# Kernel tuning notes

Measured on AMD Instinct MI355X. Metric: run time of the kernel, lower is better.

The kernel has to match this reference:

```python
import jax, jax.numpy as jnp
import numpy as np

B, T, OBS, ACT, H, S = 512, 64, 1024, 32, 1024, 64


def setup_inputs() -> dict:
    key = jax.random.key(0)
    ks = jax.random.split(key, 16)
    w = lambda k, shape: 0.02 * jax.random.normal(k, shape, jnp.float32)
    return {
        "obs": jax.random.normal(ks[0], (B, T, OBS), jnp.float32),
        "action": jax.random.normal(ks[1], (B, T, ACT), jnp.float32),
        "eps": jax.random.normal(ks[2], (B, T, S), jnp.float32),
        # obs encoder: Linear(OBS->H) + ReLU
        "W_enc": w(ks[3], (H, OBS)), "b_enc": jnp.zeros((H,), jnp.float32),
        # GRUCell(stoch+action -> H), torch gate order: r, z, n
        "W_ih": w(ks[4], (3 * H, S + ACT)), "W_hh": w(ks[5], (3 * H, H)),
        "b_ih": jnp.zeros((3 * H,), jnp.float32), "b_hh": jnp.zeros((3 * H,), jnp.float32),
        # prior: Linear(H -> 2S); posterior: Linear(2H -> 2S)
        "W_prior": w(ks[6], (2 * S, H)), "b_prior": jnp.zeros((2 * S,), jnp.float32),
        "W_post": w(ks[7], (2 * S, 2 * H)), "b_post": jnp.zeros((2 * S,), jnp.float32),
        # decoder: Linear(H+S -> H) ReLU Linear(H -> OBS)
        "W_dec1": w(ks[8], (H, H + S)), "b_dec1": jnp.zeros((H,), jnp.float32),
        "W_dec2": w(ks[9], (OBS, H)), "b_dec2": jnp.zeros((OBS,), jnp.float32),
        # reward / done heads: Linear(H+S -> 1)
        "W_rew": w(ks[10], (1, H + S)), "b_rew": jnp.zeros((1,), jnp.float32),
        "W_done": w(ks[11], (1, H + S)), "b_done": jnp.zeros((1,), jnp.float32),
    }


def _stats(x):
    mean, raw_std = jnp.split(x, 2, axis=-1)
    return mean, jax.nn.softplus(raw_std) + 1e-4


def reference(obs, action, eps, W_enc, b_enc, W_ih, W_hh, b_ih, b_hh,
              W_prior, b_prior, W_post, b_post, W_dec1, b_dec1, W_dec2, b_dec2,
              W_rew, b_rew, W_done, b_done):
    batch = obs.shape[0]
    hid = W_hh.shape[1]
    sdim = eps.shape[-1]
    # obs encoder is per-step independent -> batch it over time up front
    emb_all = jax.nn.relu(jnp.einsum('bto,ho->bth', obs, W_enc) + b_enc)

    def step(carry, xs):
        deter, stoch = carry
        a_t, emb_t, eps_t = xs
        # torch GRUCell
        x = jnp.concatenate([stoch, a_t], axis=-1)
        gi = x @ W_ih.T + b_ih
        gh = deter @ W_hh.T + b_hh
        i_r, i_z, i_n = jnp.split(gi, 3, axis=-1)
        h_r, h_z, h_n = jnp.split(gh, 3, axis=-1)
        r = jax.nn.sigmoid(i_r + h_r)
        z = jax.nn.sigmoid(i_z + h_z)
        n = jnp.tanh(i_n + r * h_n)
        deter = (1.0 - z) * n + z * deter
        # prior / posterior stats
        p_mean, p_std = _stats(deter @ W_prior.T + b_prior)
        q_mean, q_std = _stats(jnp.concatenate([deter, emb_t], axis=-1) @ W_post.T + b_post)
        stoch = q_mean + eps_t * q_std  # reparam sample
        feat = jnp.concatenate([deter, stoch], axis=-1)
        pred = jax.nn.relu(feat @ W_dec1.T + b_dec1) @ W_dec2.T + b_dec2
        rew = feat @ W_rew.T + b_rew
        done = feat @ W_done.T + b_done
        kl = jnp.log(p_std / q_std) + (q_std ** 2 + (q_mean - p_mean) ** 2) / (2.0 * p_std ** 2) - 0.5
        return (deter, stoch), (pred, rew, done, kl.mean(axis=-1, keepdims=True))

    init = (jnp.zeros((batch, hid), obs.dtype), jnp.zeros((batch, sdim), obs.dtype))
    xs = (jnp.swapaxes(action, 0, 1), jnp.swapaxes(emb_all, 0, 1), jnp.swapaxes(eps, 0, 1))
    _, (preds, rews, dones, kls) = jax.lax.scan(step, init, xs)
    pred = jnp.swapaxes(preds, 0, 1)    # [B,T,OBS]
    reward = jnp.swapaxes(rews, 0, 1)   # [B,T,1]
    done = jnp.swapaxes(dones, 0, 1)    # [B,T,1]
    kl = kls.mean()
    return pred, reward, done, kl
```

## Files before the change

kernel.cpp:

```cpp
#include <hip/hip_runtime.h>
#include <stdint.h>

#define BB 512
#define TT 64
#define OBSD 1024
#define ACTD 32
#define HD 1024
#define SD 64
#define BT (BB*TT)
#define G3 (3*HD)
#define STRD ((long)TT*HD)

typedef unsigned int uint32;
typedef unsigned long long ull;
typedef unsigned short u16;
typedef __attribute__((ext_vector_type(8))) short bf16x8;
typedef __attribute__((ext_vector_type(4))) float f32x4;

__device__ __forceinline__ float bf2f(u16 v){ uint32_t u = ((uint32_t)v)<<16; return __builtin_bit_cast(float,u); }
__device__ __forceinline__ u16 f2bf(float f){ uint32_t u = __builtin_bit_cast(uint32_t,f); uint32_t r = (u + 0x7FFFu + ((u>>16)&1u))>>16; return (u16)r; }
__device__ __forceinline__ float sigm(float x){ return 1.f/(1.f+expf(-x)); }
#define MFMA __builtin_amdgcn_mfma_f32_16x16x32_bf16

__global__ void cvt_kernel(const float* __restrict__ in, u16* __restrict__ out, long n){
  long i = (long)blockIdx.x*blockDim.x + threadIdx.x;
  long st = (long)gridDim.x*blockDim.x;
  for (; i<n; i+=st) out[i] = f2bf(in[i]);
}

struct GemmP {
  const u16* a0; const u16* a1; const u16* a2;
  const u16* b0; const u16* b1; const u16* b2;
  long lda0, lda1, lda2, ldb0, ldb1, ldb2;
  int kc0, kc1, kc2, kcPerZ;
  float* cf; u16* cb;
  long ldc, ldcb, zstride;
  const float* bias0; const float* bias1;
  int relu;
};

template<int BM,int BN>
__global__ __launch_bounds__(256) void gemm_bf16(GemmP p){
  constexpr int SA = 40;
  __shared__ u16 sA[BM*SA];
  __shared__ u16 sB[BN*SA];
  const int m0 = blockIdx.y*BM, n0 = blockIdx.x*BN;
  const int tid = threadIdx.x, lane = tid&63, wave = tid>>6;
  const int wm = (wave>>1)*(BM/2), wn = (wave&1)*(BN/2);
  constexpr int FM = BM/32, FN = BN/32;
  f32x4 acc[FM][FN] = {};
  const int cbeg = blockIdx.z*p.kcPerZ;
  int cend = cbeg + p.kcPerZ; if (cend > p.kc2) cend = p.kc2;
  const int sr = tid>>2, sc = (tid&3)*8;
  const int kg = lane>>4, lr = lane&15;
  for (int c=cbeg;c<cend;++c){
    const u16* ap; const u16* bp; long lda, ldb; int kofs;
    if (c < p.kc0){ ap=p.a0; bp=p.b0; lda=p.lda0; ldb=p.ldb0; kofs=c*32; }
    else if (c < p.kc1){ ap=p.a1; bp=p.b1; lda=p.lda1; ldb=p.ldb1; kofs=(c-p.kc0)*32; }
    else { ap=p.a2; bp=p.b2; lda=p.lda2; ldb=p.ldb2; kofs=(c-p.kc1)*32; }
    #pragma unroll
    for (int it=0; it<BM/64; ++it){
      int row = sr + it*64;
      *(bf16x8*)&sA[row*SA+sc] = *(const bf16x8*)(ap + (long)(m0+row)*lda + kofs + sc);
    }
    #pragma unroll
    for (int it=0; it<BN/64; ++it){
      int row = sr + it*64;
      *(bf16x8*)&sB[row*SA+sc] = *(const bf16x8*)(bp + (long)(n0+row)*ldb + kofs + sc);
    }
    __syncthreads();
    bf16x8 af[FM], bfv[FN];
    #pragma unroll
    for (int i=0;i<FM;++i) af[i] = *(const bf16x8*)&sA[(wm+i*16+lr)*SA + kg*8];
    #pragma unroll
    for (int j=0;j<FN;++j) bfv[j] = *(const bf16x8*)&sB[(wn+j*16+lr)*SA + kg*8];
    #pragma unroll
    for (int i=0;i<FM;++i)
      #pragma unroll
      for (int j=0;j<FN;++j)
        acc[i][j] = MFMA(af[i], bfv[j], acc[i][j], 0,0,0);
    __syncthreads();
  }
  const bool partial = (gridDim.z > 1);
  float* cf = p.cf ? (p.cf + (partial ? (long)blockIdx.z*p.zstride : 0)) : nullptr;
  #pragma unroll
  for (int i=0;i<FM;++i){
    #pragma unroll
    for (int j=0;j<FN;++j){
      const int gr0 = m0 + wm + i*16 + kg*4;
      const int gc = n0 + wn + j*16 + lr;
      float bias = 0.f;
      if (!partial){
        if (p.bias0) bias += p.bias0[gc];
        if (p.bias1) bias += p.bias1[gc];
      }
      #pragma unroll
      for (int r=0;r<4;++r){
        float v = acc[i][j][r] + bias;
        if (p.relu) v = fmaxf(v, 0.f);
        const long row = gr0 + r;
        if (cf) cf[row*p.ldc + gc] = v;
        if (p.cb) p.cb[row*p.ldcb + gc] = f2bf(v);
      }
    }
  }
}

struct ScanArgs {
  const u16* act; const u16* Wih; const u16* Whh;
  const float* b_ih; const float* b_hh;
  const u16* Wpos; const float* qemb; const float* eps;
  u16* det; u16* sto; float* qm; float* qs;
  uint32* slots;
};

__device__ __forceinline__ void gsync_g(uint32* slots, int m, int n, uint32 val){
  asm volatile("s_waitcnt vmcnt(0)" ::: "memory");
  __syncthreads();
  if (threadIdx.x == 0)
    __hip_atomic_store(&slots[m*64 + n], val, __ATOMIC_RELAXED, __HIP_MEMORY_SCOPE_AGENT);
  if (threadIdx.x < 32){
    while (__hip_atomic_load(&slots[m*64 + threadIdx.x], __ATOMIC_RELAXED,
                             __HIP_MEMORY_SCOPE_AGENT) < val)
      __builtin_amdgcn_s_sleep(2);
  }
  __syncthreads();
}

#define SA2 152

__global__ __launch_bounds__(256, 1) void scan_kernel(ScanArgs A){
  __shared__ __align__(16) u16 lds[(64+96)*SA2];
  u16* sA = lds; u16* sB = lds + 64*SA2;
  float* pf = (float*)lds;
  const int bid = blockIdx.x;
  const int tid = threadIdx.x, lane = tid&63, wave = tid>>6;
  const int lr = lane&15, kg = lane>>4;
  const int n = bid&31, m = bid>>5;
  const int m0 = m*64, h0 = n*32;
  const int wrow = (wave&1)*32, wcol = (wave>>1)*16;

  const int srow = tid>>4;
  const int scu  = (tid&15)*8;

  long whhb[6], wihb[6];
  #pragma unroll
  for (int i=0;i<6;++i){
    int br = srow + i*16;
    int gate = br>>5, hr = br&31;
    whhb[i] = (long)(gate*HD + h0 + hr)*HD + scu;
    wihb[i] = (long)(gate*HD + h0 + hr)*96 + scu;
  }

  const int h4 = h0 + wcol + kg*4;
  float bir[4], bhr[4], biz[4], bhz[4], bin[4], bhn[4];
  #pragma unroll
  for (int r=0;r<4;++r){
    bir[r]=A.b_ih[h4+r];      bhr[r]=A.b_hh[h4+r];
    biz[r]=A.b_ih[HD+h4+r];   bhz[r]=A.b_hh[HD+h4+r];
    bin[r]=A.b_ih[2*HD+h4+r]; bhn[r]=A.b_hh[2*HD+h4+r];
  }

  const int pj = n & 3, prt = n >> 2;

  float dreg[2][4] = {{0.f,0.f,0.f,0.f},{0.f,0.f,0.f,0.f}};
  const bf16x8 zerov = {};

  bf16x8 pa[4], pb[6];
  auto loadgt = [&](int tt, int g){
    if (g < 8){
      if (tt > 0){
        const u16* s = A.det + (long)(tt-1)*HD + g*128 + scu;
        #pragma unroll
        for (int j=0;j<4;++j) pa[j] = *(const bf16x8*)(s + (long)(m0+srow+16*j)*STRD);
      } else { pa[0]=zerov; pa[1]=zerov; pa[2]=zerov; pa[3]=zerov; }
      #pragma unroll
      for (int i=0;i<6;++i) pb[i] = *(const bf16x8*)(A.Whh + whhb[i] + g*128);
    } else {
      if (scu < 64){
        if (tt > 0){
          #pragma unroll
          for (int j=0;j<4;++j)
            pa[j] = *(const bf16x8*)(A.sto + (long)(m0+srow+16*j)*((long)TT*SD) + (long)(tt-1)*SD + scu);
        } else { pa[0]=zerov; pa[1]=zerov; pa[2]=zerov; pa[3]=zerov; }
      } else if (scu < 96){
        #pragma unroll
        for (int j=0;j<4;++j)
          pa[j] = *(const bf16x8*)(A.act + (long)(m0+srow+16*j)*((long)TT*ACTD) + (long)tt*ACTD + (scu-64));
      } else { pa[0]=zerov; pa[1]=zerov; pa[2]=zerov; pa[3]=zerov; }
      #pragma unroll
      for (int i=0;i<6;++i) pb[i] = (scu < 96) ? *(const bf16x8*)(A.Wih + wihb[i]) : zerov;
    }
  };

  loadgt(0, 0);
  for (int t=0; t<TT; ++t){
    f32x4 aR[2]={}, aZ[2]={}, aNd[2]={}, aNx[2]={};
    for (int g=0; g<9; ++g){
      __syncthreads();
      #pragma unroll
      for (int j=0;j<4;++j) *(bf16x8*)&sA[(srow+16*j)*SA2 + scu] = pa[j];
      #pragma unroll
      for (int i=0;i<6;++i) *(bf16x8*)&sB[(srow+16*i)*SA2 + scu] = pb[i];
      if (g < 8) loadgt(t, g+1);
      __syncthreads();
      #pragma unroll
      for (int k=0;k<4;++k){
        bf16x8 a0v = *(const bf16x8*)&sA[(wrow+lr)*SA2 + k*32 + kg*8];
        bf16x8 a1v = *(const bf16x8*)&sA[(wrow+16+lr)*SA2 + k*32 + kg*8];
        bf16x8 b0 = *(const bf16x8*)&sB[(wcol+lr)*SA2 + k*32 + kg*8];
        bf16x8 b1 = *(const bf16x8*)&sB[(32+wcol+lr)*SA2 + k*32 + kg*8];
        bf16x8 b2 = *(const bf16x8*)&sB[(64+wcol+lr)*SA2 + k*32 + kg*8];
        aR[0] = MFMA(b0,a0v,aR[0],0,0,0); aR[1] = MFMA(b0,a1v,aR[1],0,0,0);
        aZ[0] = MFMA(b1,a0v,aZ[0],0,0,0); aZ[1] = MFMA(b1,a1v,aZ[1],0,0,0);
        if (g<8){ aNd[0] = MFMA(b2,a0v,aNd[0],0,0,0); aNd[1] = MFMA(b2,a1v,aNd[1],0,0,0); }
        else    { aNx[0] = MFMA(b2,a0v,aNx[0],0,0,0); aNx[1] = MFMA(b2,a1v,aNx[1],0,0,0); }
      }
    }
    #pragma unroll
    for (int rf=0;rf<2;++rf){
      const long brow = m0 + wrow + rf*16 + lr;
      u16 pk[4];
      #pragma unroll
      for (int r=0;r<4;++r){
        float rr = sigm(aR[rf][r]+bir[r]+bhr[r]);
        float z  = sigm(aZ[rf][r]+biz[r]+bhz[r]);
        float nn = tanhf(aNx[rf][r]+bin[r] + rr*(aNd[rf][r]+bhn[r]));
        float d = (1.f - z)*nn + z*dreg[rf][r];
        dreg[rf][r] = d;
        pk[r] = f2bf(d);
      }
      ull pv; __builtin_memcpy(&pv, pk, 8);
      __hip_atomic_store((ull*)(A.det + brow*STRD + (long)t*HD + h4), pv,
                         __ATOMIC_RELAXED, __HIP_MEMORY_SCOPE_AGENT);
    }
    gsync_g(A.slots, m, n, (uint32)(2*t+1));
    {
      f32x4 accM = {}, accS = {};
      const int k0 = wave*256;
      const u16* arow = A.det + (long)(m0 + prt*8 + (lr&7))*STRD + (long)t*HD + k0 + kg*8;
      const u16* bm = A.Wpos + (long)(pj*16 + lr)*(2*HD) + k0 + kg*8;
      const u16* bs = A.Wpos + (long)(64 + pj*16 + lr)*(2*HD) + k0 + kg*8;
      #pragma unroll
      for (int kk=0; kk<8; ++kk){
        bf16x8 af = *(const bf16x8*)(arow + kk*32);
        accM = MFMA(af, *(const bf16x8*)(bm + kk*32), accM, 0,0,0);
        accS = MFMA(af, *(const bf16x8*)(bs + kk*32), accS, 0,0,0);
      }
      #pragma unroll
      for (int r=0;r<4;++r){
        int rowt = kg*4 + r;
        pf[wave*512 + rowt*16 + lr]       = accM[r];
        pf[wave*512 + 256 + rowt*16 + lr] = accS[r];
      }
      __syncthreads();
      if (tid < 64){
        const int row = tid>>3;
        const int s2 = (tid&7)*2;
        const long grow = m0 + prt*8 + row;
        const float* qe = A.qemb + grow*((long)TT*128) + (long)t*128;
        const float* ep = A.eps  + grow*((long)TT*SD) + (long)t*SD;
        u16 spk[2];
        #pragma unroll
        for (int i=0;i<2;++i){
          int sl = s2 + i, sg = pj*16 + sl;
          float mean = pf[row*16+sl] + pf[512+row*16+sl] + pf[1024+row*16+sl] + pf[1536+row*16+sl];
          float rsv  = pf[256+row*16+sl] + pf[768+row*16+sl] + pf[1280+row*16+sl] + pf[1792+row*16+sl];
          mean += qe[sg];
          rsv  += qe[64+sg];
          float sp = fmaxf(rsv,0.f) + log1pf(expf(-fabsf(rsv)));
          float qs_ = sp + 1e-4f;
          float st = mean + ep[sg]*qs_;
          A.qm[grow*((long)TT*SD) + (long)t*SD + sg] = mean;
          A.qs[grow*((long)TT*SD) + (long)t*SD + sg] = qs_;
          spk[i] = f2bf(st);
        }
        uint32 pv; __builtin_memcpy(&pv, spk, 4);
        __hip_atomic_store((uint32*)(A.sto + grow*((long)TT*SD) + (long)t*SD + pj*16 + s2), pv,
                           __ATOMIC_RELAXED, __HIP_MEMORY_SCOPE_AGENT);
      }
      __syncthreads();
    }
    if (t+1 < TT) loadgt(t+1, 0);
    gsync_g(A.slots, m, n, (uint32)(2*t+2));
  }
}

__global__ __launch_bounds__(256) void gru_step(
    const u16* __restrict__ sto_prev, long ssto,
    const u16* __restrict__ act_t,
    const u16* __restrict__ det_prev, long sdet,
    const u16* __restrict__ Wih, const u16* __restrict__ Whh,
    const float* __restrict__ b_ih, const float* __restrict__ b_hh,
    float* __restrict__ deterF, u16* __restrict__ det_bf_t){
  constexpr int SA = 40;
  __shared__ u16 sA[32*SA];
  __shared__ u16 sB[96*SA];
  const int id = blockIdx.x;
  const int n = (id&7) + ((id>>7)<<3);
  const int m = (id>>3)&15;
  const int m0 = m*32, h0 = n*32;
  const int tid = threadIdx.x, lane = tid&63, wave = tid>>6;
  const int wm = wave>>1, wn = wave&1;
  const int lr = lane&15, kg = lane>>4;

  f32x4 aR = {}, aZ = {}, aNd = {}, aNx = {};

  auto aAddr = [&](int c, int row, int sc)->const u16*{
    if (c < 32) return det_prev + (long)(m0+row)*sdet + c*32 + sc;
    if (c < 34) return sto_prev + (long)(m0+row)*ssto + (c-32)*32 + sc;
    return act_t + (long)(m0+row)*((long)TT*ACTD) + sc;
  };
  auto bAddr = [&](int c, int l)->const u16*{
    int row = l>>2, sc = (l&3)*8;
    int g = row>>5, hr = row&31;
    if (c < 32) return Whh + (long)(g*1024 + h0 + hr)*HD + c*32 + sc;
    return Wih + (long)(g*1024 + h0 + hr)*(SD+ACTD) + (c-32)*32 + sc;
  };

  bf16x8 rA, rB0, rB1;
  auto loadc = [&](int c){
    rB0 = *(const bf16x8*)bAddr(c, tid);
    if (tid < 128){
      rA  = *(const bf16x8*)aAddr(c, tid>>2, (tid&3)*8);
      rB1 = *(const bf16x8*)bAddr(c, 256+tid);
    }
  };

  loadc(0);
  for (int c=0; c<35; ++c){
    *(bf16x8*)&sB[(tid>>2)*SA + (tid&3)*8] = rB0;
    if (tid < 128){
      *(bf16x8*)&sA[(tid>>2)*SA + (tid&3)*8] = rA;
      int l = 256+tid;
      *(bf16x8*)&sB[(l>>2)*SA + (l&3)*8] = rB1;
    }
    if (c < 34) loadc(c+1);
    __syncthreads();
    bf16x8 af = *(const bf16x8*)&sA[(wm*16+lr)*SA + kg*8];
    bf16x8 b0 = *(const bf16x8*)&sB[(     wn*16+lr)*SA + kg*8];
    bf16x8 b1 = *(const bf16x8*)&sB[(32 + wn*16+lr)*SA + kg*8];
    bf16x8 b2 = *(const bf16x8*)&sB[(64 + wn*16+lr)*SA + kg*8];
    aR = MFMA(af,b0,aR,0,0,0);
    aZ = MFMA(af,b1,aZ,0,0,0);
    if (c < 32) aNd = MFMA(af,b2,aNd,0,0,0);
    else        aNx = MFMA(af,b2,aNx,0,0,0);
    __syncthreads();
  }

  const int col = h0 + wn*16 + lr;
  const float bir = b_ih[col],      bhr = b_hh[col];
  const float biz = b_ih[col+HD],   bhz = b_hh[col+HD];
  const float bin = b_ih[col+2*HD], bhn = b_hh[col+2*HD];
  #pragma unroll
  for (int reg=0; reg<4; ++reg){
    const int row = m0 + wm*16 + kg*4 + reg;
    float r = sigm(aR[reg] + bir + bhr);
    float z = sigm(aZ[reg] + biz + bhz);
    float nn = tanhf(aNx[reg] + bin + r*(aNd[reg] + bhn));
    const long fidx = (long)row*HD + col;
    float d = (1.f - z)*nn + z*deterF[fidx];
    deterF[fidx] = d;
    det_bf_t[(long)row*STRD + col] = f2bf(d);
  }
}

__global__ __launch_bounds__(256) void post_step(
    const u16* __restrict__ det_t,
    const u16* __restrict__ Wpos,
    const float* __restrict__ qemb_t,
    const float* __restrict__ eps_t,
    float* __restrict__ qm_t, float* __restrict__ qs_t, u16* __restrict__ sto_out){
  constexpr int SA = 40;
  __shared__ u16 sA4[4*16*SA];
  __shared__ u16 sB4[4*128*SA];
  const int m0 = blockIdx.x*16;
  const int tid = threadIdx.x, lane = tid&63, w = tid>>6;
  const int lr = lane&15, kg = lane>>4;

  f32x4 acc[8] = {};
  bf16x8 rA, rB[8];
  auto loadIter = [&](int i){
    #pragma unroll
    for (int rnd=0; rnd<8; ++rnd){
      int l = rnd*256 + tid;
      int q = l>>9, row = (l>>2)&127, sc = (l&3)*8;
      rB[rnd] = *(const bf16x8*)(Wpos + (long)row*(2*HD) + (q*8+i)*32 + sc);
    }
    { int q = tid>>6, row = (tid>>2)&15, sc = (tid&3)*8;
      rA = *(const bf16x8*)(det_t + (long)(m0+row)*STRD + (q*8+i)*32 + sc); }
  };

  loadIter(0);
  for (int i=0; i<8; ++i){
    #pragma unroll
    for (int rnd=0; rnd<8; ++rnd){
      int l = rnd*256 + tid;
      int q = l>>9, row = (l>>2)&127, sc = (l&3)*8;
      *(bf16x8*)&sB4[q*128*SA + row*SA + sc] = rB[rnd];
    }
    { int q = tid>>6, row = (tid>>2)&15, sc = (tid&3)*8;
      *(bf16x8*)&sA4[q*16*SA + row*SA + sc] = rA; }
    if (i < 7) loadIter(i+1);
    __syncthreads();
    bf16x8 af = *(const bf16x8*)&sA4[w*16*SA + lr*SA + kg*8];
    #pragma unroll
    for (int j=0; j<8; ++j){
      bf16x8 bf = *(const bf16x8*)&sB4[w*128*SA + (j*16+lr)*SA + kg*8];
      acc[j] = MFMA(af, bf, acc[j], 0,0,0);
    }
    __syncthreads();
  }

  float* pf = (float*)sB4;
  #pragma unroll
  for (int j=0; j<8; ++j)
    #pragma unroll
    for (int reg=0; reg<4; ++reg)
      pf[w*2048 + (kg*4+reg)*128 + j*16+lr] = acc[j][reg];
  __syncthreads();

  #pragma unroll
  for (int i=0; i<4; ++i){
    int p = tid + i*256;
    int row = p>>6, s = p&63;
    int b = m0 + row;
    float mval = pf[row*128+s]      + pf[2048+row*128+s]      + pf[4096+row*128+s]      + pf[6144+row*128+s];
    float rsv  = pf[row*128+64+s]   + pf[2048+row*128+64+s]   + pf[4096+row*128+64+s]   + pf[6144+row*128+64+s];
    mval += qemb_t[(long)b*((long)TT*128) + s];
    rsv  += qemb_t[(long)b*((long)TT*128) + 64 + s];
    float sp = fmaxf(rsv,0.f) + log1pf(expf(-fabsf(rsv)));
    float qsv = sp + 1e-4f;
    float e = eps_t[(long)b*((long)TT*SD) + s];
    float st = mval + e*qsv;
    qm_t[(long)b*((long)TT*SD) + s] = mval;
    qs_t[(long)b*((long)TT*SD) + s] = qsv;
    sto_out[(long)b*((long)TT*SD) + s] = f2bf(st);
  }
}

__global__ void kl_kernel(const float* __restrict__ pbuf, const float* __restrict__ qm,
                          const float* __restrict__ qs, float* __restrict__ klrows){
  int m = blockIdx.x*4 + (threadIdx.x>>6);
  int s = threadIdx.x & 63;
  float pm   = pbuf[(long)m*128 + s];
  float praw = pbuf[(long)m*128 + 64 + s];
  float ps = fmaxf(praw,0.f) + log1pf(expf(-fabsf(praw))) + 1e-4f;
  float qmv = qm[(long)m*64+s], qsv = qs[(long)m*64+s];
  float d = qmv - pm;
  float kl = logf(ps/qsv) + (qsv*qsv + d*d)/(2.f*ps*ps) - 0.5f;
  #pragma unroll
  for (int off=32; off; off>>=1) kl += __shfl_xor(kl, off);
  if (s==0) klrows[m] = kl*(1.f/64.f);
}

__global__ void kl_reduce(const float* __restrict__ klrows, float* __restrict__ out){
  __shared__ float sm[256];
  float a = 0.f;
  for (int i=threadIdx.x; i<BT; i+=256) a += klrows[i];
  sm[threadIdx.x]=a; __syncthreads();
  for (int off=128; off; off>>=1){ if ((int)threadIdx.x<off) sm[threadIdx.x]+=sm[threadIdx.x+off]; __syncthreads(); }
  if (threadIdx.x==0) out[0] = sm[0] / (float)BT;
}

__global__ void rewdone_kernel(const u16* __restrict__ det, const u16* __restrict__ sto,
    const float* __restrict__ Wr, const float* __restrict__ br,
    const float* __restrict__ Wd, const float* __restrict__ bd,
    float* __restrict__ orew, float* __restrict__ odone){
  int m = blockIdx.x*4 + (threadIdx.x>>6);
  int lane = threadIdx.x & 63;
  float ar=0.f, ad=0.f;
  for (int k=lane; k<HD+SD; k+=64){
    float f = (k<HD) ? bf2f(det[(long)m*HD+k]) : bf2f(sto[(long)m*SD + (k-HD)]);
    ar = fmaf(f, Wr[k], ar); ad = fmaf(f, Wd[k], ad);
  }
  #pragma unroll
  for (int off=32; off; off>>=1){ ar += __shfl_xor(ar, off); ad += __shfl_xor(ad, off); }
  if (lane==0){ orew[m]=ar+br[0]; odone[m]=ad+bd[0]; }
}

static char* carve(char*& base, size_t bytes){
  char* p = base; base += (bytes + 255) & ~(size_t)255; return p;
}

extern "C" void kernel_launch(void* const* d_in, const int* in_sizes, int n_in,
                              void* d_out, int out_size, void* d_ws, size_t ws_size,
                              hipStream_t stream) {
  const float* obs    = (const float*)d_in[0];
  const float* action = (const float*)d_in[1];
  const float* eps    = (const float*)d_in[2];
  const float* W_enc  = (const float*)d_in[3];
  const float* b_enc  = (const float*)d_in[4];
  const float* W_ih   = (const float*)d_in[5];
  const float* W_hh   = (const float*)d_in[6];
  const float* b_ih   = (const float*)d_in[7];
  const float* b_hh   = (const float*)d_in[8];
  const float* W_prior= (const float*)d_in[9];
  const float* b_prior= (const float*)d_in[10];
  const float* W_post = (const float*)d_in[11];
  const float* b_post = (const float*)d_in[12];
  const float* W_dec1 = (const float*)d_in[13];
  const float* b_dec1 = (const float*)d_in[14];
  const float* W_dec2 = (const float*)d_in[15];
  const float* b_dec2 = (const float*)d_in[16];
  const float* W_rew  = (const float*)d_in[17];
  const float* b_rew  = (const float*)d_in[18];
  const float* W_done = (const float*)d_in[19];
  const float* b_done = (const float*)d_in[20];

  char* w = (char*)d_ws;
  u16* obs_bf  = (u16*)carve(w, (size_t)BT*OBSD*2);
  u16* emb_bf  = (u16*)carve(w, (size_t)BT*HD*2);
  u16* det_bf  = (u16*)carve(w, (size_t)BT*HD*2);
  u16* sto_bf  = (u16*)carve(w, (size_t)BT*SD*2);
  u16* act_bf  = (u16*)carve(w, (size_t)BT*ACTD*2);
  u16* Wenc_bf = (u16*)carve(w, (size_t)HD*OBSD*2);
  u16* Wih_bf  = (u16*)carve(w, (size_t)G3*(SD+ACTD)*2);
  u16* Whh_bf  = (u16*)carve(w, (size_t)G3*HD*2);
  u16* Wpri_bf = (u16*)carve(w, (size_t)2*SD*HD*2);
  u16* Wpos_bf = (u16*)carve(w, (size_t)2*SD*2*HD*2);
  u16* Wd1_bf  = (u16*)carve(w, (size_t)HD*(HD+SD)*2);
  u16* Wd2_bf  = (u16*)carve(w, (size_t)OBSD*HD*2);
  u16* zero_bf = (u16*)carve(w, 4096);
  float* deterF = (float*)carve(w, (size_t)BB*HD*4);
  float* qemb   = (float*)carve(w, (size_t)BT*128*4);
  float* qm_all = (float*)carve(w, (size_t)BT*SD*4);
  float* qs_all = (float*)carve(w, (size_t)BT*SD*4);
  float* p_buf  = (float*)carve(w, (size_t)BT*2*SD*4);
  float* klrows = (float*)carve(w, (size_t)BT*4);
  uint32* syncb = (uint32*)carve(w, 4096);
  u16* hid_bf = obs_bf;

  if ((size_t)(w - (char*)d_ws) > ws_size){
    hipMemsetAsync(d_out, 0xFF, 4, stream);
    return;
  }

  auto cvt = [&](const float* in, u16* out, long n){
    cvt_kernel<<<dim3(2048), dim3(256), 0, stream>>>(in, out, n);
  };
  cvt(obs, obs_bf, (long)BT*OBSD);
  cvt(action, act_bf, (long)BT*ACTD);
  cvt(W_enc, Wenc_bf, (long)HD*OBSD);
  cvt(W_ih, Wih_bf, (long)G3*(SD+ACTD));
  cvt(W_hh, Whh_bf, (long)G3*HD);
  cvt(W_prior, Wpri_bf, (long)2*SD*HD);
  cvt(W_post, Wpos_bf, (long)2*SD*2*HD);
  cvt(W_dec1, Wd1_bf, (long)HD*(HD+SD));
  cvt(W_dec2, Wd2_bf, (long)OBSD*HD);
  hipMemsetAsync(zero_bf, 0, 4096, stream);
  hipMemsetAsync(deterF, 0, (size_t)BB*HD*4, stream);
  hipMemsetAsync(syncb, 0, 4096, stream);

  {
    GemmP q{};
    q.a0 = obs_bf;  q.lda0 = OBSD;
    q.b0 = Wenc_bf; q.ldb0 = OBSD;
    q.kc0=q.kc1=q.kc2=32; q.kcPerZ=32;
    q.cb = emb_bf; q.ldcb = HD;
    q.bias0 = b_enc; q.relu = 1;
    gemm_bf16<128,128><<<dim3(HD/128, BT/128, 1), 256, 0, stream>>>(q);
  }
  {
    GemmP q{};
    q.a0 = emb_bf;       q.lda0 = HD;
    q.b0 = Wpos_bf + HD; q.ldb0 = 2*HD;
    q.kc0=q.kc1=q.kc2=32; q.kcPerZ=32;
    q.cf = qemb; q.ldc = 128;
    q.bias0 = b_post;
    gemm_bf16<64,64><<<dim3(128/64, BT/64, 1), 256, 0, stream>>>(q);
  }

  {
    ScanArgs sa;
    sa.act = act_bf; sa.Wih = Wih_bf; sa.Whh = Whh_bf;
    sa.b_ih = b_ih; sa.b_hh = b_hh;
    sa.Wpos = Wpos_bf; sa.qemb = qemb; sa.eps = eps;
    sa.det = det_bf; sa.sto = sto_bf; sa.qm = qm_all; sa.qs = qs_all;
    sa.slots = syncb;
    void* kargs[] = { (void*)&sa };
    hipError_t cerr = hipLaunchCooperativeKernel((const void*)scan_kernel,
        dim3(256), dim3(256), kargs, 0, stream);
    if (cerr != hipSuccess){
      for (int t=0; t<TT; ++t){
        const u16* sto_p = (t==0) ? zero_bf : (sto_bf + (long)(t-1)*SD);
        long ssto        = (t==0) ? 0 : (long)TT*SD;
        const u16* det_p = (t==0) ? zero_bf : (det_bf + (long)(t-1)*HD);
        long sdet        = (t==0) ? 0 : STRD;
        gru_step<<<dim3(512), 256, 0, stream>>>(sto_p, ssto, act_bf + (long)t*ACTD,
            det_p, sdet, Wih_bf, Whh_bf, b_ih, b_hh, deterF, det_bf + (long)t*HD);
        post_step<<<dim3(32), 256, 0, stream>>>(det_bf + (long)t*HD, Wpos_bf,
            qemb + (long)t*128, eps + (long)t*SD,
            qm_all + (long)t*SD, qs_all + (long)t*SD, sto_bf + (long)t*SD);
      }
    }
  }

  {
    GemmP q{};
    q.a0 = det_bf;  q.lda0 = HD;
    q.b0 = Wpri_bf; q.ldb0 = HD;
    q.kc0=q.kc1=q.kc2=32; q.kcPerZ=32;
    q.cf = p_buf; q.ldc = 2*SD;
    q.bias0 = b_prior;
    gemm_bf16<64,64><<<dim3(2*SD/64, BT/64, 1), 256, 0, stream>>>(q);
  }
  kl_kernel<<<dim3(BT/4), 256, 0, stream>>>(p_buf, qm_all, qs_all, klrows);
  {
    GemmP q{};
    q.a0 = det_bf; q.lda0 = HD;
    q.a1 = sto_bf; q.lda1 = SD;
    q.b0 = Wd1_bf;      q.ldb0 = HD+SD;
    q.b1 = Wd1_bf + HD; q.ldb1 = HD+SD;
    q.kc0=32; q.kc1=34; q.kc2=34; q.kcPerZ=34;
    q.cb = hid_bf; q.ldcb = HD;
    q.bias0 = b_dec1; q.relu = 1;
    gemm_bf16<128,128><<<dim3(HD/128, BT/128, 1), 256, 0, stream>>>(q);
  }
  {
    GemmP q{};
    q.a0 = hid_bf; q.lda0 = HD;
    q.b0 = Wd2_bf; q.ldb0 = HD;
    q.kc0=q.kc1=q.kc2=32; q.kcPerZ=32;
    q.cf = (float*)d_out; q.ldc = OBSD;
    q.bias0 = b_dec2;
    gemm_bf16<128,128><<<dim3(OBSD/128, BT/128, 1), 256, 0, stream>>>(q);
  }
  rewdone_kernel<<<dim3(BT/4), 256, 0, stream>>>(det_bf, sto_bf, W_rew, b_rew, W_done, b_done,
      (float*)d_out + (long)BT*OBSD, (float*)d_out + (long)BT*OBSD + BT);
  kl_reduce<<<dim3(1), 256, 0, stream>>>(klrows, (float*)d_out + (long)BT*OBSD + 2*BT);
}
```

Measured before the change: 1.701 ms.

## Defer second grid barrier until stoch is needed in next step's input gates

Replaces the full barrier after the posterior/stoch phase with a one-sided flag publish. The matching wait is moved into the next step's gate loop, just before the Wih chunk that reads the previous stoch. This lets the eight Whh chunks of step t+1 (which depend only on deter) overlap with slower peers finishing the posterior. Two separate slot arrays with monotone step counters replace the shared counter, and the sync buffer is enlarged. The cost is more complex ordering logic and a risk of subtle memory-visibility races.

New measurement: 1.770 ms. 4.0% more time.

```diff
diff --git a/kernel.cpp b/kernel.cpp
--- a/kernel.cpp
+++ b/kernel.cpp
@@ -114,19 +114,6 @@
   uint32* slots;
 };
 
-__device__ __forceinline__ void gsync_g(uint32* slots, int m, int n, uint32 val){
-  asm volatile("s_waitcnt vmcnt(0)" ::: "memory");
-  __syncthreads();
-  if (threadIdx.x == 0)
-    __hip_atomic_store(&slots[m*64 + n], val, __ATOMIC_RELAXED, __HIP_MEMORY_SCOPE_AGENT);
-  if (threadIdx.x < 32){
-    while (__hip_atomic_load(&slots[m*64 + threadIdx.x], __ATOMIC_RELAXED,
-                             __HIP_MEMORY_SCOPE_AGENT) < val)
-      __builtin_amdgcn_s_sleep(2);
-  }
-  __syncthreads();
-}
-
 #define SA2 152
 
 __global__ __launch_bounds__(256, 1) void scan_kernel(ScanArgs A){
@@ -142,6 +129,9 @@
 
   const int srow = tid>>4;
   const int scu  = (tid&15)*8;
+
+  uint32* slots1 = A.slots;
+  uint32* slots2 = A.slots + 512;
 
   long whhb[6], wihb[6];
   #pragma unroll
@@ -193,8 +183,7 @@
     }
   };
 
-  loadgt(0, 0);
-  for (int t=0; t<TT; ++t){
+  auto gates = [&](int tt){
     f32x4 aR[2]={}, aZ[2]={}, aNd[2]={}, aNx[2]={};
     for (int g=0; g<9; ++g){
       __syncthreads();
@@ -202,7 +191,16 @@
       for (int j=0;j<4;++j) *(bf16x8*)&sA[(srow+16*j)*SA2 + scu] = pa[j];
       #pragma unroll
       for (int i=0;i<6;++i) *(bf16x8*)&sB[(srow+16*i)*SA2 + scu] = pb[i];
-      if (g < 8) loadgt(t, g+1);
+      if (g < 7) loadgt(tt, g+1);
+      else if (g == 7){
+        if (tid < 32){
+          while (__hip_atomic_load(&slots2[m*64 + tid], __ATOMIC_RELAXED,
+                                   __HIP_MEMORY_SCOPE_AGENT) < (uint32)tt)
+            __builtin_amdgcn_s_sleep(2);
+        }
+        __syncthreads();
+        loadgt(tt, 8);
+      }
       __syncthreads();
       #pragma unroll
       for (int k=0;k<4;++k){
@@ -231,10 +229,26 @@
         pk[r] = f2bf(d);
       }
       ull pv; __builtin_memcpy(&pv, pk, 8);
-      __hip_atomic_store((ull*)(A.det + brow*STRD + (long)t*HD + h4), pv,
+      __hip_atomic_store((ull*)(A.det + brow*STRD + (long)tt*HD + h4), pv,
                          __ATOMIC_RELAXED, __HIP_MEMORY_SCOPE_AGENT);
     }
-    gsync_g(A.slots, m, n, (uint32)(2*t+1));
+    asm volatile("s_waitcnt vmcnt(0)" ::: "memory");
+    __syncthreads();
+    if (tid == 0)
+      __hip_atomic_store(&slots1[m*64 + n], (uint32)(tt+1), __ATOMIC_RELAXED,
+                         __HIP_MEMORY_SCOPE_AGENT);
+    if (tid < 32){
+      while (__hip_atomic_load(&slots1[m*64 + tid], __ATOMIC_RELAXED,
+                               __HIP_MEMORY_SCOPE_AGENT) < (uint32)(tt+1))
+        __builtin_amdgcn_s_sleep(2);
+    }
+    __syncthreads();
+  };
+
+  loadgt(0, 0);
+  gates(0);
+  for (int t=0; t<TT; ++t){
+    if (t+1 < TT) loadgt(t+1, 0);
     {
       f32x4 accM = {}, accS = {};
       const int k0 = wave*256;
@@ -279,10 +293,13 @@
         __hip_atomic_store((uint32*)(A.sto + grow*((long)TT*SD) + (long)t*SD + pj*16 + s2), pv,
                            __ATOMIC_RELAXED, __HIP_MEMORY_SCOPE_AGENT);
       }
-      __syncthreads();
-    }
-    if (t+1 < TT) loadgt(t+1, 0);
-    gsync_g(A.slots, m, n, (uint32)(2*t+2));
+    }
+    asm volatile("s_waitcnt vmcnt(0)" ::: "memory");
+    __syncthreads();
+    if (tid == 0)
+      __hip_atomic_store(&slots2[m*64 + n], (uint32)(t+1), __ATOMIC_RELAXED,
+                         __HIP_MEMORY_SCOPE_AGENT);
+    if (t+1 < TT) gates(t+1);
   }
 }
 
@@ -528,7 +545,7 @@
   float* qs_all = (float*)carve(w, (size_t)BT*SD*4);
   float* p_buf  = (float*)carve(w, (size_t)BT*2*SD*4);
   float* klrows = (float*)carve(w, (size_t)BT*4);
-  uint32* syncb = (uint32*)carve(w, 4096);
+  uint32* syncb = (uint32*)carve(w, 8192);
   u16* hid_bf = obs_bf;
 
   if ((size_t)(w - (char*)d_ws) > ws_size){
@@ -550,7 +567,7 @@
   cvt(W_dec2, Wd2_bf, (long)OBSD*HD);
   hipMemsetAsync(zero_bf, 0, 4096, stream);
   hipMemsetAsync(deterF, 0, (size_t)BB*HD*4, stream);
-  hipMemsetAsync(syncb, 0, 4096, stream);
+  hipMemsetAsync(syncb, 0, 8192, stream);
 
   {
     GemmP q{};
```

## Double-buffer GEMM tiles with direct global-to-LDS async loads

Applied to the files above, without the earlier changes.

The bf16 GEMM kernel now stages A/B tiles straight into LDS using global_load_lds, skipping the round trip through registers. Two LDS buffers let the next K-chunk load while MFMAs run on the current one. The LDS row padding is removed, so stride-32 rows may cause bank conflicts on fragment reads. The sync buffer size is also enlarged.

Result: no change. 1.672 ms (-1.7%).

```diff
diff --git a/kernel.cpp b/kernel.cpp
--- a/kernel.cpp
+++ b/kernel.cpp
@@ -21,6 +21,12 @@
 __device__ __forceinline__ u16 f2bf(float f){ uint32_t u = __builtin_bit_cast(uint32_t,f); uint32_t r = (u + 0x7FFFu + ((u>>16)&1u))>>16; return (u16)r; }
 __device__ __forceinline__ float sigm(float x){ return 1.f/(1.f+expf(-x)); }
 #define MFMA __builtin_amdgcn_mfma_f32_16x16x32_bf16
+
+__device__ __forceinline__ void gload16(const u16* g, u16* l){
+  __builtin_amdgcn_global_load_lds(
+      (const __attribute__((address_space(1))) u16*)g,
+      (__attribute__((address_space(3))) u16*)l, 16, 0, 0);
+}
 
 __global__ void cvt_kernel(const float* __restrict__ in, u16* __restrict__ out, long n){
   long i = (long)blockIdx.x*blockDim.x + threadIdx.x;
@@ -41,9 +47,7 @@
 
 template<int BM,int BN>
 __global__ __launch_bounds__(256) void gemm_bf16(GemmP p){
-  constexpr int SA = 40;
-  __shared__ u16 sA[BM*SA];
-  __shared__ u16 sB[BN*SA];
+  __shared__ __align__(16) u16 sAB[2][(BM+BN)*32];
   const int m0 = blockIdx.y*BM, n0 = blockIdx.x*BN;
   const int tid = threadIdx.x, lane = tid&63, wave = tid>>6;
   const int wm = (wave>>1)*(BM/2), wn = (wave&1)*(BN/2);
@@ -51,29 +55,42 @@
   f32x4 acc[FM][FN] = {};
   const int cbeg = blockIdx.z*p.kcPerZ;
   int cend = cbeg + p.kcPerZ; if (cend > p.kc2) cend = p.kc2;
-  const int sr = tid>>2, sc = (tid&3)*8;
   const int kg = lane>>4, lr = lane&15;
-  for (int c=cbeg;c<cend;++c){
+  const int srow = lane>>2, scol = (lane&3)*8;
+
+  auto STAGE = [&](int buf, int c){
     const u16* ap; const u16* bp; long lda, ldb; int kofs;
     if (c < p.kc0){ ap=p.a0; bp=p.b0; lda=p.lda0; ldb=p.ldb0; kofs=c*32; }
     else if (c < p.kc1){ ap=p.a1; bp=p.b1; lda=p.lda1; ldb=p.ldb1; kofs=(c-p.kc0)*32; }
     else { ap=p.a2; bp=p.b2; lda=p.lda2; ldb=p.ldb2; kofs=(c-p.kc1)*32; }
+    u16* base = sAB[buf];
     #pragma unroll
     for (int it=0; it<BM/64; ++it){
-      int row = sr + it*64;
-      *(bf16x8*)&sA[row*SA+sc] = *(const bf16x8*)(ap + (long)(m0+row)*lda + kofs + sc);
+      int row = it*64 + wave*16 + srow;
+      gload16(ap + (long)(m0+row)*lda + kofs + scol,
+              base + (it*64 + wave*16)*32);
     }
     #pragma unroll
     for (int it=0; it<BN/64; ++it){
-      int row = sr + it*64;
-      *(bf16x8*)&sB[row*SA+sc] = *(const bf16x8*)(bp + (long)(n0+row)*ldb + kofs + sc);
-    }
+      int row = it*64 + wave*16 + srow;
+      gload16(bp + (long)(n0+row)*ldb + kofs + scol,
+              base + BM*32 + (it*64 + wave*16)*32);
+    }
+  };
+
+  STAGE(0, cbeg);
+  for (int c=cbeg;c<cend;++c){
+    const int cur = (c-cbeg)&1;
+    asm volatile("s_waitcnt vmcnt(0)" ::: "memory");
     __syncthreads();
+    if (c+1 < cend) STAGE(cur^1, c+1);
+    const u16* sA = sAB[cur];
+    const u16* sB = sAB[cur] + BM*32;
     bf16x8 af[FM], bfv[FN];
     #pragma unroll
-    for (int i=0;i<FM;++i) af[i] = *(const bf16x8*)&sA[(wm+i*16+lr)*SA + kg*8];
-    #pragma unroll
-    for (int j=0;j<FN;++j) bfv[j] = *(const bf16x8*)&sB[(wn+j*16+lr)*SA + kg*8];
+    for (int i=0;i<FM;++i) af[i] = *(const bf16x8*)&sA[(wm+i*16+lr)*32 + kg*8];
+    #pragma unroll
+    for (int j=0;j<FN;++j) bfv[j] = *(const bf16x8*)&sB[(wn+j*16+lr)*32 + kg*8];
     #pragma unroll
     for (int i=0;i<FM;++i)
       #pragma unroll
@@ -528,7 +545,7 @@
   float* qs_all = (float*)carve(w, (size_t)BT*SD*4);
   float* p_buf  = (float*)carve(w, (size_t)BT*2*SD*4);
   float* klrows = (float*)carve(w, (size_t)BT*4);
-  uint32* syncb = (uint32*)carve(w, 4096);
+  uint32* syncb = (uint32*)carve(w, 8192);
   u16* hid_bf = obs_bf;
 
   if ((size_t)(w - (char*)d_ws) > ws_size){
@@ -550,7 +567,7 @@
   cvt(W_dec2, Wd2_bf, (long)OBSD*HD);
   hipMemsetAsync(zero_bf, 0, 4096, stream);
   hipMemsetAsync(deterF, 0, (size_t)BB*HD*4, stream);
-  hipMemsetAsync(syncb, 0, 4096, stream);
+  hipMemsetAsync(syncb, 0, 8192, stream);
 
   {
     GemmP q{};
```
